# Kernel tuning notes

Measured on AMD Instinct MI355X. Metric: run time of the kernel, lower is better.

The kernel has to match this reference:

```python
import jax, jax.numpy as jnp
import numpy as np

N = 100000          # number of road-network nodes
E = 640000          # number of directed edges (sparse adjacency nnz)
HID = 128           # hidden_dims = lane(16)+type(32)+length(16)+node(64)
N_LAYERS = 3        # hparams.baseline_gat_layer


def setup_inputs() -> dict:
    key = jax.random.key(0)
    ks = jax.random.split(key, 12)
    inp = {
        'node_feature': jax.random.randint(ks[0], (N,), 0, 100000),
        'type_feature': jax.random.randint(ks[1], (N,), 0, 20),
        'length_feature': jax.random.randint(ks[2], (N,), 0, 100),
        'lane_feature': jax.random.randint(ks[3], (N,), 0, 10),
        'adj_src': jax.random.randint(ks[4], (E,), 0, N),
        'adj_dst': jax.random.randint(ks[5], (E,), 0, N),
        'adj_val': jax.random.uniform(ks[6], (E,), dtype=jnp.float32),
        # learned parameters
        'node_emb': jax.random.normal(ks[7], (100000, 64), dtype=jnp.float32) * 0.02,
        'type_emb': jax.random.normal(ks[8], (20, 32), dtype=jnp.float32) * 0.02,
        'length_emb': jax.random.normal(ks[9], (100, 16), dtype=jnp.float32) * 0.02,
        'lane_emb': jax.random.normal(ks[10], (10, 16), dtype=jnp.float32) * 0.02,
        'W': jax.random.normal(ks[11], (HID, HID), dtype=jnp.float32) / np.sqrt(HID),
        'b': jnp.zeros((HID,), dtype=jnp.float32),
    }
    return inp


def spgcn_layer(x, W, b, adj_src, adj_dst, adj_val):
    # GCN layer: out = spmm(adj, x @ W) + b, adj given as COO edge list
    support = x @ W                                # [N, HID]
    msg = support[adj_src] * adj_val[:, None]      # gather + scale, [E, HID]
    agg = jax.ops.segment_sum(msg, adj_dst, num_segments=N)  # scatter-add
    return agg + b


def reference(node_feature, type_feature, length_feature, lane_feature,
              adj_src, adj_dst, adj_val,
              node_emb, type_emb, length_emb, lane_emb, W, b):
    # embedding lookups + concat: [lane, type, length, node] -> [N, HID]
    raw_feat = jnp.concatenate([
        lane_emb[lane_feature],
        type_emb[type_feature],
        length_emb[length_feature],
        node_emb[node_feature],
    ], axis=1)
    # repeated propagation with the SAME shared SPGCN layer weights
    for _ in range(N_LAYERS):
        raw_feat = spgcn_layer(raw_feat, W, b, adj_src, adj_dst, adj_val)
    return raw_feat
```

## Files before the change

### kernel.cpp

```cpp
#include <hip/hip_runtime.h>
#include <hip/hip_bf16.h>

typedef __hip_bfloat16 bf16;
typedef unsigned short ushort_t;
typedef __attribute__((ext_vector_type(8))) short short8;
typedef __attribute__((ext_vector_type(4))) float f32x4;

#define NN 100000
#define NE 640000
#define HD 128
#define NB 391
#define EMB_U 6250
#define HIST_U 2500
#define GEMM_U 1563
#define AGG_U 6250
#define D_U 391
#define LDA 136


__device__ __forceinline__ float bf2f(ushort_t u) {
    unsigned v = (unsigned)u << 16;
    return __builtin_bit_cast(float, v);
}
__device__ __forceinline__ ushort_t f2bf(float f) {
    bf16 h = __float2bfloat16(f);
    return *(ushort_t*)&h;
}

struct P {
    const int *nodef, *typef, *lenf, *lanef, *adj_src, *adj_dst;
    const float *adj_val, *node_emb, *type_emb, *len_emb, *lane_emb, *W, *bias;
    ushort_t *Xa, *Xb, *w2t, *w3t;
    float *bw, *bw2, *d, *d2;
    int *cnt, *offs, *slots, *bsum;
    int2 *epack;
    float *outf;
};

__global__ __launch_bounds__(256) void ehist_k(P p) {
    __shared__ ushort_t WtL[HD * HD];
    __shared__ float bwS[HD];
    const int tid = threadIdx.x;
    if (blockIdx.x >= 1 + HIST_U) {
        const int idx = (blockIdx.x - 1 - HIST_U) * 256 + tid;
        const int i = idx >> 4;
        const int c = (idx & 15) * 8;
        const float* tbl; size_t base;
        if (c < 16)      { tbl = p.lane_emb; base = (size_t)p.lanef[i] * 16 + c; }
        else if (c < 48) { tbl = p.type_emb; base = (size_t)p.typef[i] * 32 + (c - 16); }
        else if (c < 64) { tbl = p.len_emb;  base = (size_t)p.lenf[i]  * 16 + (c - 48); }
        else             { tbl = p.node_emb; base = (size_t)p.nodef[i] * 64 + (c - 64); }
        const float4 f0 = *(const float4*)(tbl + base);
        const float4 f1 = *(const float4*)(tbl + base + 4);
        ushort_t u8[8] = { f2bf(f0.x), f2bf(f0.y), f2bf(f0.z), f2bf(f0.w),
                           f2bf(f1.x), f2bf(f1.y), f2bf(f1.z), f2bf(f1.w) };
        *(uint4*)(p.Xa + (size_t)i * HD + c) = *(uint4*)u8;
        return;
    }
    if (blockIdx.x >= 1) {
        const int e = (blockIdx.x - 1) * 256 + tid;
        p.slots[e] = atomicAdd(&p.cnt[p.adj_dst[e]], 1);
        return;
    }
    for (int i = tid; i < HD * HD / 4; i += 256) {
        const int k  = (i * 4) >> 7;
        const int n0 = (i * 4) & 127;
        const float4 f = *(const float4*)&p.W[(size_t)k * HD + n0];
        WtL[(n0 + 0) * HD + k] = f2bf(f.x);
        WtL[(n0 + 1) * HD + k] = f2bf(f.y);
        WtL[(n0 + 2) * HD + k] = f2bf(f.z);
        WtL[(n0 + 3) * HD + k] = f2bf(f.w);
    }
    __syncthreads();

    const int w = tid >> 6;
    const int ln = tid & 15;
    const int quad = (tid >> 4) & 3;
    const int koff = quad * 8;
    const f32x4 zero = {0.f, 0.f, 0.f, 0.f};

    short8 bfrg[2][4];
#pragma unroll
    for (int nt = 0; nt < 2; ++nt)
#pragma unroll
        for (int kc = 0; kc < 4; ++kc)
            bfrg[nt][kc] = *(const short8*)&WtL[(w * 32 + nt * 16 + ln) * HD + kc * 32 + koff];

#pragma unroll
    for (int mt = 0; mt < 8; ++mt) {
        const int m = mt * 16 + ln;
        short8 afrg[4];
#pragma unroll
        for (int kc = 0; kc < 4; ++kc) {
            ushort_t a[8];
#pragma unroll
            for (int j = 0; j < 8; ++j)
                a[j] = WtL[(kc * 32 + koff + j) * HD + m];
            afrg[kc] = *(short8*)a;
        }
        f32x4 acc[2] = {zero, zero};
#pragma unroll
        for (int nt = 0; nt < 2; ++nt)
#pragma unroll
            for (int kc = 0; kc < 4; ++kc)
                acc[nt] = __builtin_amdgcn_mfma_f32_16x16x32_bf16(
                        afrg[kc], bfrg[nt][kc], acc[nt], 0, 0, 0);
#pragma unroll
        for (int nt = 0; nt < 2; ++nt)
#pragma unroll
            for (int reg = 0; reg < 4; ++reg) {
                const int col = w * 32 + nt * 16 + ln;
                const int row = mt * 16 + quad * 4 + reg;
                p.w2t[col * HD + row] = f2bf(acc[nt][reg]);
            }
    }
    __syncthreads();

#pragma unroll
    for (int mt = 0; mt < 8; ++mt) {
        const int m = mt * 16 + ln;
        short8 afrg[4];
#pragma unroll
        for (int kc = 0; kc < 4; ++kc) {
            ushort_t a[8];
#pragma unroll
            for (int j = 0; j < 8; ++j)
                a[j] = p.w2t[(kc * 32 + koff + j) * HD + m];
            afrg[kc] = *(short8*)a;
        }
        f32x4 acc[2] = {zero, zero};
#pragma unroll
        for (int nt = 0; nt < 2; ++nt)
#pragma unroll
            for (int kc = 0; kc < 4; ++kc)
                acc[nt] = __builtin_amdgcn_mfma_f32_16x16x32_bf16(
                        afrg[kc], bfrg[nt][kc], acc[nt], 0, 0, 0);
#pragma unroll
        for (int nt = 0; nt < 2; ++nt)
#pragma unroll
            for (int reg = 0; reg < 4; ++reg) {
                const int col = w * 32 + nt * 16 + ln;
                const int row = mt * 16 + quad * 4 + reg;
                p.w3t[col * HD + row] = f2bf(acc[nt][reg]);
            }
    }
    __syncthreads();

    if (tid < HD) {
        float s = 0.f;
        for (int k = 0; k < HD; ++k) s += p.bias[k] * bf2f(WtL[tid * HD + k]);
        bwS[tid] = s;
        p.bw[tid] = s;
    }
    __syncthreads();
    if (tid < HD) {
        float s = 0.f;
        for (int k = 0; k < HD; ++k) s += bwS[k] * bf2f(WtL[tid * HD + k]);
        p.bw2[tid] = s;
    }
}


__global__ __launch_bounds__(256) void scan1_k(P p) {
    __shared__ int s[256];
    const int tid = threadIdx.x;
    const int idx = blockIdx.x * 256 + tid;
    s[tid] = (idx < NN) ? p.cnt[idx] : 0;
    __syncthreads();
    for (int o = 128; o; o >>= 1) {
        if (tid < o) s[tid] += s[tid + o];
        __syncthreads();
    }
    if (tid == 0) p.bsum[blockIdx.x] = s[0];
}

__global__ __launch_bounds__(256) void scan3_k(P p) {
    __shared__ int s[256];
    const int b = blockIdx.x;
    const int tid = threadIdx.x;
    int acc = 0;
    for (int i = tid; i < b; i += 256) acc += p.bsum[i];
    s[tid] = acc;
    __syncthreads();
    for (int o = 128; o; o >>= 1) {
        if (tid < o) s[tid] += s[tid + o];
        __syncthreads();
    }
    const int boffv = s[0];
    __syncthreads();
    const int idx = b * 256 + tid;
    int v = (idx < NN) ? p.cnt[idx] : 0;
    s[tid] = v;
    __syncthreads();
    for (int o = 1; o < 256; o <<= 1) {
        int x = (tid >= o) ? s[tid - o] : 0;
        __syncthreads();
        s[tid] += x;
        __syncthreads();
    }
    const int excl = s[tid] - v + boffv;
    if (idx <= NN) p.offs[idx] = excl;
}

__global__ __launch_bounds__(256) void pos_k(P p) {
    const int e = blockIdx.x * 256 + threadIdx.x;
    const int dst = p.adj_dst[e];
    int2 pk;
    pk.x = p.adj_src[e];
    pk.y = __float_as_int(p.adj_val[e]);
    p.epack[p.offs[dst] + p.slots[e]] = pk;
}

__global__ __launch_bounds__(256) void agg_k(P p, const ushort_t* __restrict__ Xin,
                                             ushort_t* __restrict__ Xout, int aux) {
    if (blockIdx.x >= AGG_U) {
        const int node = (blockIdx.x - AGG_U) * 256 + threadIdx.x;
        if (node < NN) {
            const int lo = p.offs[node], hi = p.offs[node + 1];
            float s = 0.f;
            if (aux == 1) {
                for (int j = lo; j < hi; ++j) s += __int_as_float(p.epack[j].y);
                p.d[node] = s;
            } else {
                for (int j = lo; j < hi; ++j) {
                    const int2 e = p.epack[j];
                    s += __int_as_float(e.y) * p.d[e.x];
                }
                p.d2[node] = s;
            }
        }
        return;
    }
    const int node = blockIdx.x * 16 + (threadIdx.x >> 4);
    const int lane = threadIdx.x & 15;
    const int c = lane * 8;
    const int lo = p.offs[node];
    const int hi = p.offs[node + 1];
    float a0[8], a1[8], a2[8], a3[8];
#pragma unroll
    for (int k = 0; k < 8; ++k) { a0[k] = a1[k] = a2[k] = a3[k] = 0.f; }
    int j = lo;
    for (; j + 3 < hi; j += 4) {
        const int2 e0 = p.epack[j], e1 = p.epack[j + 1];
        const int2 e2 = p.epack[j + 2], e3 = p.epack[j + 3];
        const short8 u0 = *(const short8*)(Xin + (size_t)e0.x * HD + c);
        const short8 u1 = *(const short8*)(Xin + (size_t)e1.x * HD + c);
        const short8 u2 = *(const short8*)(Xin + (size_t)e2.x * HD + c);
        const short8 u3 = *(const short8*)(Xin + (size_t)e3.x * HD + c);
        const float v0 = __int_as_float(e0.y), v1 = __int_as_float(e1.y);
        const float v2 = __int_as_float(e2.y), v3 = __int_as_float(e3.y);
#pragma unroll
        for (int k = 0; k < 8; ++k) {
            a0[k] += bf2f((ushort_t)u0[k]) * v0;
            a1[k] += bf2f((ushort_t)u1[k]) * v1;
            a2[k] += bf2f((ushort_t)u2[k]) * v2;
            a3[k] += bf2f((ushort_t)u3[k]) * v3;
        }
    }
    for (; j < hi; ++j) {
        const int2 e0 = p.epack[j];
        const float v0 = __int_as_float(e0.y);
        const short8 u0 = *(const short8*)(Xin + (size_t)e0.x * HD + c);
#pragma unroll
        for (int k = 0; k < 8; ++k) a0[k] += bf2f((ushort_t)u0[k]) * v0;
    }
    ushort_t u8[8];
#pragma unroll
    for (int k = 0; k < 8; ++k) u8[k] = f2bf((a0[k] + a1[k]) + (a2[k] + a3[k]));
    *(uint4*)(Xout + (size_t)node * HD + c) = *(uint4*)u8;
}

__global__ __launch_bounds__(256) void gemmf_k(P p, const ushort_t* __restrict__ X2) {
    __shared__ ushort_t Xs[64 * LDA];
    const int tid = threadIdx.x;
    const int row0 = blockIdx.x * 64;

    {
        const int g = tid >> 4;
        const int lane = tid & 15;
        const int c = lane * 8;
#pragma unroll
        for (int mi = 0; mi < 4; ++mi) {
            const int m = g * 4 + mi;
            const int gm = row0 + m;
            float a0[8], a1[8], a2[8], a3[8];
#pragma unroll
            for (int k = 0; k < 8; ++k) { a0[k] = a1[k] = a2[k] = a3[k] = 0.f; }
            if (gm < NN) {
                const int lo = p.offs[gm];
                const int hi = p.offs[gm + 1];
                int j = lo;
                for (; j + 3 < hi; j += 4) {
                    const int2 e0 = p.epack[j], e1 = p.epack[j + 1];
                    const int2 e2 = p.epack[j + 2], e3 = p.epack[j + 3];
                    const short8 u0 = *(const short8*)(X2 + (size_t)e0.x * HD + c);
                    const short8 u1 = *(const short8*)(X2 + (size_t)e1.x * HD + c);
                    const short8 u2 = *(const short8*)(X2 + (size_t)e2.x * HD + c);
                    const short8 u3 = *(const short8*)(X2 + (size_t)e3.x * HD + c);
                    const float v0 = __int_as_float(e0.y), v1 = __int_as_float(e1.y);
                    const float v2 = __int_as_float(e2.y), v3 = __int_as_float(e3.y);
#pragma unroll
                    for (int k = 0; k < 8; ++k) {
                        a0[k] += bf2f((ushort_t)u0[k]) * v0;
                        a1[k] += bf2f((ushort_t)u1[k]) * v1;
                        a2[k] += bf2f((ushort_t)u2[k]) * v2;
                        a3[k] += bf2f((ushort_t)u3[k]) * v3;
                    }
                }
                for (; j < hi; ++j) {
                    const int2 e0 = p.epack[j];
                    const float v0 = __int_as_float(e0.y);
                    const short8 u0 = *(const short8*)(X2 + (size_t)e0.x * HD + c);
#pragma unroll
                    for (int k = 0; k < 8; ++k) a0[k] += bf2f((ushort_t)u0[k]) * v0;
                }
            }
            ushort_t u8[8];
#pragma unroll
            for (int k = 0; k < 8; ++k) u8[k] = f2bf((a0[k] + a1[k]) + (a2[k] + a3[k]));
            *(uint4*)&Xs[m * LDA + c] = *(uint4*)u8;
        }
    }

    const int w = tid >> 6;
    const int ln = tid & 15;
    const int quad = (tid >> 4) & 3;
    const int koff = quad * 8;
    const int col0 = w * 32 + ln;
    const int col1 = col0 + 16;

    short8 bfrg[2][4];
#pragma unroll
    for (int nt = 0; nt < 2; ++nt)
#pragma unroll
        for (int kc = 0; kc < 4; ++kc)
            bfrg[nt][kc] = *(const short8*)&p.w3t[(size_t)(w * 32 + nt * 16 + ln) * HD + kc * 32 + koff];

    const float bwc0 = p.bw[col0],  bwc1 = p.bw[col1];
    const float bw2c0 = p.bw2[col0], bw2c1 = p.bw2[col1];
    const float bc0 = p.bias[col0], bc1 = p.bias[col1];

    __syncthreads();

    const f32x4 zero = {0.f, 0.f, 0.f, 0.f};
#pragma unroll
    for (int mt = 0; mt < 4; ++mt) {
        short8 afrg[4];
#pragma unroll
        for (int kc = 0; kc < 4; ++kc)
            afrg[kc] = *(const short8*)&Xs[(mt * 16 + ln) * LDA + kc * 32 + koff];
        f32x4 acc[2] = {zero, zero};
#pragma unroll
        for (int nt = 0; nt < 2; ++nt)
#pragma unroll
            for (int kc = 0; kc < 4; ++kc)
                acc[nt] = __builtin_amdgcn_mfma_f32_16x16x32_bf16(
                        afrg[kc], bfrg[nt][kc], acc[nt], 0, 0, 0);
#pragma unroll
        for (int reg = 0; reg < 4; ++reg) {
            const int gm = row0 + mt * 16 + quad * 4 + reg;
            if (gm < NN) {
                const float dg = p.d[gm], d2g = p.d2[gm];
                p.outf[(size_t)gm * HD + col0] = acc[0][reg] + d2g * bw2c0 + dg * bwc0 + bc0;
                p.outf[(size_t)gm * HD + col1] = acc[1][reg] + d2g * bw2c1 + dg * bwc1 + bc1;
            }
        }
    }
}

extern "C" void kernel_launch(void* const* d_in, const int* in_sizes, int n_in,
                              void* d_out, int out_size, void* d_ws, size_t ws_size,
                              hipStream_t stream) {
    P p;
    p.nodef    = (const int*)d_in[0];
    p.typef    = (const int*)d_in[1];
    p.lenf     = (const int*)d_in[2];
    p.lanef    = (const int*)d_in[3];
    p.adj_src  = (const int*)d_in[4];
    p.adj_dst  = (const int*)d_in[5];
    p.adj_val  = (const float*)d_in[6];
    p.node_emb = (const float*)d_in[7];
    p.type_emb = (const float*)d_in[8];
    p.len_emb  = (const float*)d_in[9];
    p.lane_emb = (const float*)d_in[10];
    p.W        = (const float*)d_in[11];
    p.bias     = (const float*)d_in[12];
    p.outf     = (float*)d_out;

    const size_t xbytes = (size_t)NN * HD * 2;
    char* wp = (char*)d_ws;
    p.Xa    = (ushort_t*)wp; wp += xbytes;
    p.Xb    = (ushort_t*)wp; wp += xbytes;
    p.cnt   = (int*)wp;      wp += (size_t)NN * 4;
    p.offs  = (int*)wp;      wp += 400016;
    p.slots = (int*)wp;      wp += (size_t)NE * 4;
    p.epack = (int2*)wp;     wp += (size_t)NE * 8;
    p.w2t   = (ushort_t*)wp; wp += 32768;
    p.w3t   = (ushort_t*)wp; wp += 32768;
    p.bw    = (float*)wp;    wp += 512;
    p.bw2   = (float*)wp;    wp += 512;
    p.d     = (float*)wp;    wp += (size_t)NN * 4;
    p.d2    = (float*)wp;    wp += (size_t)NN * 4;
    p.bsum  = (int*)wp;      wp += 1600;

    hipMemsetAsync(p.cnt, 0, (size_t)NN * 4, stream);
    ehist_k<<<1 + HIST_U + EMB_U, 256, 0, stream>>>(p);
    scan1_k<<<NB, 256, 0, stream>>>(p);
    scan3_k<<<NB, 256, 0, stream>>>(p);
    pos_k<<<HIST_U, 256, 0, stream>>>(p);
    agg_k<<<AGG_U + D_U, 256, 0, stream>>>(p, p.Xa, p.Xb, 1);
    agg_k<<<AGG_U + D_U, 256, 0, stream>>>(p, p.Xb, p.Xa, 2);
    gemmf_k<<<GEMM_U, 256, 0, stream>>>(p, p.Xa);
}
```

Baseline: 292.0 us.

## Replace two-pass scan with atomic per-wave offsets; double GEMM row tile

The two-kernel block scan that built CSR offsets is replaced by one kernel: each wavefront does a shuffle prefix sum and reserves its base with an atomicAdd on a global counter. Node segments are then no longer in node order, so consumers compute hi from offs+cnt instead of offs[node+1]. The fused aggregation+GEMM kernel also processes 128 rows per block instead of 64, halving block count. This removes one launch and a serial block-offset pass, but gives less locality in the edge array and fewer, heavier GEMM blocks.

```diff
diff --git a/kernel.cpp b/kernel.cpp
--- a/kernel.cpp
+++ b/kernel.cpp
@@ -12,7 +12,7 @@
 #define NB 391
 #define EMB_U 6250
 #define HIST_U 2500
-#define GEMM_U 1563
+#define GEMM_U 782
 #define AGG_U 6250
 #define D_U 391
 #define LDA 136
@@ -32,7 +32,7 @@
     const float *adj_val, *node_emb, *type_emb, *len_emb, *lane_emb, *W, *bias;
     ushort_t *Xa, *Xb, *w2t, *w3t;
     float *bw, *bw2, *d, *d2;
-    int *cnt, *offs, *slots, *bsum;
+    int *cnt, *gtot, *offs, *slots;
     int2 *epack;
     float *outf;
 };
@@ -160,46 +160,20 @@
     }
 }
 
-
-__global__ __launch_bounds__(256) void scan1_k(P p) {
-    __shared__ int s[256];
-    const int tid = threadIdx.x;
-    const int idx = blockIdx.x * 256 + tid;
-    s[tid] = (idx < NN) ? p.cnt[idx] : 0;
-    __syncthreads();
-    for (int o = 128; o; o >>= 1) {
-        if (tid < o) s[tid] += s[tid + o];
-        __syncthreads();
-    }
-    if (tid == 0) p.bsum[blockIdx.x] = s[0];
-}
-
-__global__ __launch_bounds__(256) void scan3_k(P p) {
-    __shared__ int s[256];
-    const int b = blockIdx.x;
-    const int tid = threadIdx.x;
-    int acc = 0;
-    for (int i = tid; i < b; i += 256) acc += p.bsum[i];
-    s[tid] = acc;
-    __syncthreads();
-    for (int o = 128; o; o >>= 1) {
-        if (tid < o) s[tid] += s[tid + o];
-        __syncthreads();
-    }
-    const int boffv = s[0];
-    __syncthreads();
-    const int idx = b * 256 + tid;
-    int v = (idx < NN) ? p.cnt[idx] : 0;
-    s[tid] = v;
-    __syncthreads();
-    for (int o = 1; o < 256; o <<= 1) {
-        int x = (tid >= o) ? s[tid - o] : 0;
-        __syncthreads();
-        s[tid] += x;
-        __syncthreads();
-    }
-    const int excl = s[tid] - v + boffv;
-    if (idx <= NN) p.offs[idx] = excl;
+__global__ __launch_bounds__(256) void offs_k(P p) {
+    const int idx = blockIdx.x * 256 + threadIdx.x;
+    const int lane = threadIdx.x & 63;
+    const int c = (idx < NN) ? p.cnt[idx] : 0;
+    int pf = c;
+#pragma unroll
+    for (int o = 1; o < 64; o <<= 1) {
+        const int x = __shfl_up(pf, o);
+        if (lane >= o) pf += x;
+    }
+    int base = 0;
+    if (lane == 63) base = atomicAdd(p.gtot, pf);
+    base = __shfl(base, 63);
+    if (idx < NN) p.offs[idx] = base + pf - c;
 }
 
 __global__ __launch_bounds__(256) void pos_k(P p) {
@@ -216,7 +190,7 @@
     if (blockIdx.x >= AGG_U) {
         const int node = (blockIdx.x - AGG_U) * 256 + threadIdx.x;
         if (node < NN) {
-            const int lo = p.offs[node], hi = p.offs[node + 1];
+            const int lo = p.offs[node], hi = lo + p.cnt[node];
             float s = 0.f;
             if (aux == 1) {
                 for (int j = lo; j < hi; ++j) s += __int_as_float(p.epack[j].y);
@@ -235,7 +209,7 @@
     const int lane = threadIdx.x & 15;
     const int c = lane * 8;
     const int lo = p.offs[node];
-    const int hi = p.offs[node + 1];
+    const int hi = lo + p.cnt[node];
     float a0[8], a1[8], a2[8], a3[8];
 #pragma unroll
     for (int k = 0; k < 8; ++k) { a0[k] = a1[k] = a2[k] = a3[k] = 0.f; }
@@ -271,24 +245,23 @@
 }
 
 __global__ __launch_bounds__(256) void gemmf_k(P p, const ushort_t* __restrict__ X2) {
-    __shared__ ushort_t Xs[64 * LDA];
+    __shared__ ushort_t Xs[128 * LDA];
     const int tid = threadIdx.x;
-    const int row0 = blockIdx.x * 64;
+    const int row0 = blockIdx.x * 128;
 
     {
         const int g = tid >> 4;
         const int lane = tid & 15;
         const int c = lane * 8;
-#pragma unroll
-        for (int mi = 0; mi < 4; ++mi) {
-            const int m = g * 4 + mi;
+        for (int mi = 0; mi < 8; ++mi) {
+            const int m = g * 8 + mi;
             const int gm = row0 + m;
             float a0[8], a1[8], a2[8], a3[8];
 #pragma unroll
             for (int k = 0; k < 8; ++k) { a0[k] = a1[k] = a2[k] = a3[k] = 0.f; }
             if (gm < NN) {
                 const int lo = p.offs[gm];
-                const int hi = p.offs[gm + 1];
+                const int hi = lo + p.cnt[gm];
                 int j = lo;
                 for (; j + 3 < hi; j += 4) {
                     const int2 e0 = p.epack[j], e1 = p.epack[j + 1];
@@ -344,7 +317,7 @@
 
     const f32x4 zero = {0.f, 0.f, 0.f, 0.f};
 #pragma unroll
-    for (int mt = 0; mt < 4; ++mt) {
+    for (int mt = 0; mt < 8; ++mt) {
         short8 afrg[4];
 #pragma unroll
         for (int kc = 0; kc < 4; ++kc)
@@ -392,6 +365,7 @@
     p.Xa    = (ushort_t*)wp; wp += xbytes;
     p.Xb    = (ushort_t*)wp; wp += xbytes;
     p.cnt   = (int*)wp;      wp += (size_t)NN * 4;
+    p.gtot  = (int*)wp;      wp += 16;
     p.offs  = (int*)wp;      wp += 400016;
     p.slots = (int*)wp;      wp += (size_t)NE * 4;
     p.epack = (int2*)wp;     wp += (size_t)NE * 8;
@@ -401,12 +375,10 @@
     p.bw2   = (float*)wp;    wp += 512;
     p.d     = (float*)wp;    wp += (size_t)NN * 4;
     p.d2    = (float*)wp;    wp += (size_t)NN * 4;
-    p.bsum  = (int*)wp;      wp += 1600;
-
-    hipMemsetAsync(p.cnt, 0, (size_t)NN * 4, stream);
+
+    hipMemsetAsync(p.cnt, 0, (size_t)NN * 4 + 16, stream);
     ehist_k<<<1 + HIST_U + EMB_U, 256, 0, stream>>>(p);
-    scan1_k<<<NB, 256, 0, stream>>>(p);
-    scan3_k<<<NB, 256, 0, stream>>>(p);
+    offs_k<<<NB, 256, 0, stream>>>(p);
     pos_k<<<HIST_U, 256, 0, stream>>>(p);
     agg_k<<<AGG_U + D_U, 256, 0, stream>>>(p, p.Xa, p.Xb, 1);
     agg_k<<<AGG_U + D_U, 256, 0, stream>>>(p, p.Xb, p.Xa, 2);
```

Measured after the change: 304.4 us. 4.2% more time.
